# Kernel tuning notes

Measured on AMD Instinct MI355X. Metric: run time of the kernel, lower is better.

The kernel has to match this reference:

```python
import jax, jax.numpy as jnp
import numpy as np
import math

EPS = 1e-5
L2_EPS = 1e-12  # torch F.normalize default eps


def _bitlinear(x, W):
    """BitNet b1.58-style BitLinear: ternary weights (per-tensor mean-abs scale)
    and per-token int8 absmax activation quantization. No bias.
    x: [..., in], W: [out, in] -> [..., out]
    """
    w_scale = jnp.clip(jnp.mean(jnp.abs(W)), EPS, None)
    W_q = jnp.clip(jnp.round(W / w_scale), -1.0, 1.0) * w_scale
    x_scale = 127.0 / jnp.clip(jnp.max(jnp.abs(x), axis=-1, keepdims=True), EPS, None)
    x_q = jnp.clip(jnp.round(x * x_scale), -128.0, 127.0) / x_scale
    return jnp.einsum('bsi,oi->bso', x_q, W_q)


def setup_inputs() -> dict:
    key = jax.random.key(0)
    k1, k2, k3 = jax.random.split(key, 3)
    B, S, D_in, P, D_out = 4, 4096, 2048, 16, 2048
    x = jax.random.normal(k1, (B, S, D_in), dtype=jnp.float32)
    # xavier_normal_: std = sqrt(2 / (fan_in + fan_out))
    Wk = jax.random.normal(k2, (P, D_in), dtype=jnp.float32) * math.sqrt(2.0 / (D_in + P))
    Wv = jax.random.normal(k3, (D_out, P), dtype=jnp.float32) * math.sqrt(2.0 / (P + D_out))
    return {"x": x, "Wk": Wk, "Wv": Wv}


def reference(x, Wk, Wv):
    # key projection -> [B, S, P]
    attn = _bitlinear(x, Wk)
    # gelu (exact erf form, torch default) + L2-normalize * sqrt(P)
    attn = jax.nn.gelu(attn, approximate=False)
    norm = jnp.clip(jnp.linalg.norm(attn, axis=-1, keepdims=True), L2_EPS, None)
    attn = attn / norm * jnp.sqrt(jnp.float32(attn.shape[-1]))
    # value projection -> [B, S, D_out]
    return _bitlinear(attn, Wv)
```

## Files before the change

### kernel.cpp

```cpp
#include <hip/hip_runtime.h>

#define DIN   2048
#define DOUT  2048
#define NP    16
#define TPW   4
#define WPB   4

#define HDR_OFF   0
#define WK4_OFF   256
#define WV4_OFF   (WK4_OFF + 32768)

static __device__ __forceinline__ int dot4(unsigned a, unsigned b, int c) {
#if defined(__has_builtin) && __has_builtin(__builtin_amdgcn_sdot4)
  return __builtin_amdgcn_sdot4((int)a, (int)b, c, false);
#else
  c += (int)(signed char)(a & 0xffu)        * (int)(signed char)(b & 0xffu);
  c += (int)(signed char)((a >> 8) & 0xffu) * (int)(signed char)((b >> 8) & 0xffu);
  c += (int)(signed char)((a >> 16) & 0xffu)* (int)(signed char)((b >> 16) & 0xffu);
  c += (int)(signed char)(a >> 24)          * (int)(signed char)(b >> 24);
  return c;
#endif
}

static __device__ __forceinline__ unsigned qmagic(float f, float xs) {
  return __float_as_uint(fmaf(f, xs, 12582912.0f)) & 0xffu;
}

static __device__ __forceinline__ unsigned q8(float f, float xs) {
  float t = f * xs;
  float r = rintf(t);
  r = fmaxf(-128.0f, fminf(127.0f, r));
  return ((unsigned)(int)r) & 0xffu;
}

__global__ __launch_bounds__(256) void k_prep(
    const float* __restrict__ Wk, const float* __restrict__ Wv,
    float* __restrict__ hdr, unsigned* __restrict__ wk4, unsigned* __restrict__ wv4)
{
  __shared__ float red[8][256];
  const int tid = threadIdx.x, b = blockIdx.x;
  const int isV = (b >= 32);
  const float4* W = (const float4*)(isV ? Wv : Wk);

  float4 own = make_float4(0.f, 0.f, 0.f, 0.f);
#pragma unroll
  for (int lb = 0; lb < 8; ++lb) {
    float s = 0.f;
#pragma unroll
    for (int i = 0; i < 4; ++i) {
      float4 v = W[lb * 1024 + i * 256 + tid];
      if (!isV && (lb * 4 + i) == b) own = v;
      s += fabsf(v.x) + fabsf(v.y) + fabsf(v.z) + fabsf(v.w);
    }
    red[lb][tid] = s;
  }
  __syncthreads();
#pragma unroll 1
  for (int o = 128; o > 0; o >>= 1) {
    if (tid < o) {
#pragma unroll
      for (int lb = 0; lb < 8; ++lb) red[lb][tid] += red[lb][tid + o];
    }
    __syncthreads();
  }
  float sum = 0.f;
#pragma unroll
  for (int lb = 0; lb < 8; ++lb) sum += red[lb][0];
  const float sc = fmaxf(sum * (1.0f / 32768.0f), 1e-5f);
  if (tid == 0 && (b == 0 || b == 32)) hdr[isV] = sc;

  if (!isV) {
    const int c = b * 256 + tid;
    unsigned pk = 0; const float* wp = &own.x;
#pragma unroll
    for (int j = 0; j < 4; ++j) {
      float r = rintf(wp[j] / sc);
      r = fmaxf(-1.0f, fminf(1.0f, r));
      pk |= (((unsigned)(int)r) & 0xffu) << (8 * j);
    }
    wk4[c] = pk;
  } else {
    const int o = (b - 32) * 256 + tid;
    unsigned u[4];
#pragma unroll
    for (int cc = 0; cc < 4; ++cc) {
      float4 w = ((const float4*)Wv)[o * 4 + cc];
      const float* wp = &w.x;
      unsigned pk = 0;
#pragma unroll
      for (int r = 0; r < 4; ++r) {
        float q = rintf(wp[r] / sc);
        q = fmaxf(-1.0f, fminf(1.0f, q));
        pk |= (((unsigned)(int)q) & 0xffu) << (8 * r);
      }
      u[cc] = pk;
    }
    const int m = o >> 8, r = o & 255, lr = r >> 2, j = r & 3;
    ((uint4*)wv4)[(m * 4 + j) * 64 + lr] = make_uint4(u[0], u[1], u[2], u[3]);
  }
}

__global__ __launch_bounds__(256, 4) void k_main(
    const float* __restrict__ x, const float* __restrict__ hdr,
    const unsigned* __restrict__ wk4, const unsigned* __restrict__ wv4t,
    float* __restrict__ out)
{
  const int tid = threadIdx.x;
  const int l   = tid & 63;
  const int ws  = tid >> 6;
  const long t0 = ((long)blockIdx.x * WPB + ws) * TPW;

  __shared__ uint4 wkL[2048];
  __shared__ uint4 qls[WPB][TPW];
  __shared__ float sls[WPB][TPW];

  const float w1 = hdr[0], w2 = hdr[1];
  const float4* xf  = (const float4*)x;
  const uint4*  wvt = (const uint4*)wv4t;

#pragma unroll 1
  for (int r = 0; r < 8; ++r) {
    const int d = r * 256 + tid;
    const int p = d >> 7, half = (d >> 6) & 1, lg = d & 63;
    const int s = p * 512 + half * 256 + lg;
    wkL[d] = make_uint4(wk4[s], wk4[s + 64], wk4[s + 128], wk4[s + 192]);
  }
  __syncthreads();

#pragma unroll 1
  for (int t = 0; t < TPW; ++t) {
    const long tok = t0 + t;

    float4 a[8];
#pragma unroll
    for (int c = 0; c < 8; ++c) a[c] = xf[tok * 512 + c * 64 + l];

    float mx = 0.0f;
#pragma unroll
    for (int c = 0; c < 8; ++c) {
      mx = fmaxf(mx, fabsf(a[c].x)); mx = fmaxf(mx, fabsf(a[c].y));
      mx = fmaxf(mx, fabsf(a[c].z)); mx = fmaxf(mx, fabsf(a[c].w));
    }
#pragma unroll
    for (int d = 1; d < 64; d <<= 1) mx = fmaxf(mx, __shfl_xor(mx, d, 64));
    const float mcl = fmaxf(mx, 1e-5f);
    const float xs  = 127.0f / mcl;
    const float s1  = w1 / xs;

    unsigned qp[8];
#pragma unroll
    for (int c = 0; c < 8; ++c) {
      qp[c] = qmagic(a[c].x, xs) | (qmagic(a[c].y, xs) << 8)
            | (qmagic(a[c].z, xs) << 16) | (qmagic(a[c].w, xs) << 24);
    }

    int acc[16];
#pragma unroll
    for (int p = 0; p < 16; ++p) {
      const uint4 w0 = wkL[p * 128 + l];
      const uint4 w4 = wkL[p * 128 + 64 + l];
      int d = 0;
      d = dot4(qp[0], w0.x, d); d = dot4(qp[1], w0.y, d);
      d = dot4(qp[2], w0.z, d); d = dot4(qp[3], w0.w, d);
      d = dot4(qp[4], w4.x, d); d = dot4(qp[5], w4.y, d);
      d = dot4(qp[6], w4.z, d); d = dot4(qp[7], w4.w, d);
      acc[p] = d;
    }

#pragma unroll
    for (int b = 0; b < 4; ++b) {
      const int lb = (l >> b) & 1;
#pragma unroll
      for (int j = 0; j < 8; ++j) {
        if (j < (8 >> b)) {
          int keep = lb ? acc[2 * j + 1] : acc[2 * j];
          int send = lb ? acc[2 * j]     : acc[2 * j + 1];
          acc[j] = keep + __shfl_xor(send, 1 << b, 64);
        }
      }
    }
    int rr = acc[0];
    rr += __shfl_xor(rr, 16, 64);
    rr += __shfl_xor(rr, 32, 64);

    const float fa = (float)rr * s1;
    const float gv = 0.5f * fa * (1.0f + erff(fa * 0.70710678118654752f));
    float ss = gv * gv;
    ss += __shfl_xor(ss, 1, 64); ss += __shfl_xor(ss, 2, 64);
    ss += __shfl_xor(ss, 4, 64); ss += __shfl_xor(ss, 8, 64);
    const float rn = fmaxf(sqrtf(ss), 1e-12f);
    const float gn = gv * (4.0f / rn);
    float am = fabsf(gn);
    {
      float o;
      o = __shfl_xor(am, 1, 64); am = fmaxf(am, o);
      o = __shfl_xor(am, 2, 64); am = fmaxf(am, o);
      o = __shfl_xor(am, 4, 64); am = fmaxf(am, o);
      o = __shfl_xor(am, 8, 64); am = fmaxf(am, o);
    }
    const float mc2 = fmaxf(am, 1e-5f);
    const float xs2 = 127.0f / mc2;
    const float s2  = w2 / xs2;

    unsigned sh = q8(gn, xs2) << ((l & 3) * 8);
    sh |= (unsigned)__shfl_xor((int)sh, 1, 64);
    sh |= (unsigned)__shfl_xor((int)sh, 2, 64);
    const unsigned wa = (unsigned)__shfl_xor((int)sh, 4, 64);
    const unsigned wb = (unsigned)__shfl_xor((int)sh, 8, 64);
    const unsigned wc = (unsigned)__shfl_xor((int)sh, 12, 64);
    if (l == 0) {
      qls[ws][t] = make_uint4(sh, wa, wb, wc);
      sls[ws][t] = s2;
    }
  }

  uint4 q[TPW]; float s2v[TPW];
#pragma unroll
  for (int i = 0; i < TPW; ++i) { q[i] = qls[ws][i]; s2v[i] = sls[ws][i]; }

#pragma unroll 1
  for (int m = 0; m < 8; ++m) {
    const uint4 wv0 = wvt[(m * 4 + 0) * 64 + l];
    const uint4 wv1 = wvt[(m * 4 + 1) * 64 + l];
    const uint4 wv2 = wvt[(m * 4 + 2) * 64 + l];
    const uint4 wv3 = wvt[(m * 4 + 3) * 64 + l];
#pragma unroll
    for (int t = 0; t < TPW; ++t) {
      float h[4];
      {
        int d = dot4(q[t].x, wv0.x, 0);
        d = dot4(q[t].y, wv0.y, d); d = dot4(q[t].z, wv0.z, d);
        d = dot4(q[t].w, wv0.w, d); h[0] = (float)d * s2v[t];
      }
      {
        int d = dot4(q[t].x, wv1.x, 0);
        d = dot4(q[t].y, wv1.y, d); d = dot4(q[t].z, wv1.z, d);
        d = dot4(q[t].w, wv1.w, d); h[1] = (float)d * s2v[t];
      }
      {
        int d = dot4(q[t].x, wv2.x, 0);
        d = dot4(q[t].y, wv2.y, d); d = dot4(q[t].z, wv2.z, d);
        d = dot4(q[t].w, wv2.w, d); h[2] = (float)d * s2v[t];
      }
      {
        int d = dot4(q[t].x, wv3.x, 0);
        d = dot4(q[t].y, wv3.y, d); d = dot4(q[t].z, wv3.z, d);
        d = dot4(q[t].w, wv3.w, d); h[3] = (float)d * s2v[t];
      }
      *(float4*)(out + (size_t)(t0 + t) * 2048 + m * 256 + l * 4) =
          make_float4(h[0], h[1], h[2], h[3]);
    }
  }
}

extern "C" void kernel_launch(void* const* d_in, const int* in_sizes, int n_in,
                              void* d_out, int out_size, void* d_ws, size_t ws_size,
                              hipStream_t stream) {
  const float* x  = (const float*)d_in[0];
  const float* Wk = (const float*)d_in[1];
  const float* Wv = (const float*)d_in[2];

  const int tokens = in_sizes[0] / DIN;

  char* ws = (char*)d_ws;
  float*    hdr = (float*)(ws + HDR_OFF);
  unsigned* wk4 = (unsigned*)(ws + WK4_OFF);
  unsigned* wv4 = (unsigned*)(ws + WV4_OFF);

  k_prep<<<40, 256, 0, stream>>>(Wk, Wv, hdr, wk4, wv4);
  k_main<<<tokens / (TPW * WPB), 256, 0, stream>>>(x, hdr, wk4, wv4, (float*)d_out);
}
```

Measured before the change: 297.8 us.

## Split fused BitLinear kernel into quantize, key-projection and value-projection kernels

The single fused kernel is replaced by three kernels. The first quantizes x to int8 and writes the result plus per-token scales to workspace. The second computes the 16-wide key projection, GELU, normalization and requantization with a different thread mapping: per-thread partial dots are reduced through shared memory instead of many wave shuffles. The third computes the output projection with a separate grid over output column blocks. This adds a 32 MB int8 write and read-back of x plus two extra launches, in exchange for simpler, more parallel stages.

```diff
diff --git a/kernel.cpp b/kernel.cpp
--- a/kernel.cpp
+++ b/kernel.cpp
@@ -3,12 +3,14 @@
 #define DIN   2048
 #define DOUT  2048
 #define NP    16
-#define TPW   4
-#define WPB   4
 
 #define HDR_OFF   0
 #define WK4_OFF   256
 #define WV4_OFF   (WK4_OFF + 32768)
+#define XSW_OFF   (WV4_OFF + 32768)
+#define XQ_OFF    (XSW_OFF + 65536)
+#define Q2_OFF    (XQ_OFF + 33554432)
+#define S2_OFF    (Q2_OFF + 262144)
 
 static __device__ __forceinline__ int dot4(unsigned a, unsigned b, int c) {
 #if defined(__has_builtin) && __has_builtin(__builtin_amdgcn_sdot4)
@@ -100,37 +102,17 @@
   }
 }
 
-__global__ __launch_bounds__(256, 4) void k_main(
-    const float* __restrict__ x, const float* __restrict__ hdr,
-    const unsigned* __restrict__ wk4, const unsigned* __restrict__ wv4t,
-    float* __restrict__ out)
-{
-  const int tid = threadIdx.x;
-  const int l   = tid & 63;
-  const int ws  = tid >> 6;
-  const long t0 = ((long)blockIdx.x * WPB + ws) * TPW;
-
-  __shared__ uint4 wkL[2048];
-  __shared__ uint4 qls[WPB][TPW];
-  __shared__ float sls[WPB][TPW];
-
-  const float w1 = hdr[0], w2 = hdr[1];
-  const float4* xf  = (const float4*)x;
-  const uint4*  wvt = (const uint4*)wv4t;
-
-#pragma unroll 1
-  for (int r = 0; r < 8; ++r) {
-    const int d = r * 256 + tid;
-    const int p = d >> 7, half = (d >> 6) & 1, lg = d & 63;
-    const int s = p * 512 + half * 256 + lg;
-    wkL[d] = make_uint4(wk4[s], wk4[s + 64], wk4[s + 128], wk4[s + 192]);
-  }
-  __syncthreads();
-
-#pragma unroll 1
-  for (int t = 0; t < TPW; ++t) {
-    const long tok = t0 + t;
-
+__global__ __launch_bounds__(256) void k_quant(
+    const float* __restrict__ x, unsigned* __restrict__ xqw,
+    float* __restrict__ xsw)
+{
+  const int tid = threadIdx.x, l = tid & 63, wv = tid >> 6;
+  const long tb = (long)blockIdx.x * 16 + wv * 4;
+  const float4* xf = (const float4*)x;
+
+#pragma unroll 1
+  for (int i = 0; i < 4; ++i) {
+    const long tok = tb + i;
     float4 a[8];
 #pragma unroll
     for (int c = 0; c < 8; ++c) a[c] = xf[tok * 512 + c * 64 + l];
@@ -145,111 +127,133 @@
     for (int d = 1; d < 64; d <<= 1) mx = fmaxf(mx, __shfl_xor(mx, d, 64));
     const float mcl = fmaxf(mx, 1e-5f);
     const float xs  = 127.0f / mcl;
-    const float s1  = w1 / xs;
-
-    unsigned qp[8];
+
 #pragma unroll
     for (int c = 0; c < 8; ++c) {
-      qp[c] = qmagic(a[c].x, xs) | (qmagic(a[c].y, xs) << 8)
-            | (qmagic(a[c].z, xs) << 16) | (qmagic(a[c].w, xs) << 24);
-    }
-
-    int acc[16];
+      const unsigned q = qmagic(a[c].x, xs) | (qmagic(a[c].y, xs) << 8)
+                       | (qmagic(a[c].z, xs) << 16) | (qmagic(a[c].w, xs) << 24);
+      xqw[tok * 512 + c * 64 + l] = q;
+    }
+    if (l == 0) xsw[tok] = xs;
+  }
+}
+
+__global__ __launch_bounds__(256) void k_mid(
+    const unsigned* __restrict__ xq, const float* __restrict__ xsw,
+    const unsigned* __restrict__ wk4, const float* __restrict__ hdr,
+    uint4* __restrict__ q2w, float* __restrict__ s2w)
+{
+  __shared__ unsigned wkS[8192];
+  __shared__ int accS[4][32][17];
+
+  const int tid = threadIdx.x, l = tid & 63, wv = tid >> 6;
+  const long t0 = (long)blockIdx.x * 32;
+
+#pragma unroll 1
+  for (int i = 0; i < 32; ++i) wkS[i * 256 + tid] = wk4[i * 256 + tid];
+  __syncthreads();
+
+  const int t = l >> 1, h = l & 1;
+  const unsigned* xrow = xq + (t0 + t) * 512 + wv * 128 + h * 64;
+  const unsigned* wbase = wkS + wv * 128 + h * 64;
+
+  int acc[16];
+#pragma unroll
+  for (int p = 0; p < 16; ++p) acc[p] = 0;
+
+#pragma unroll 2
+  for (int c4 = 0; c4 < 16; ++c4) {
+    const uint4 xv = *(const uint4*)(xrow + c4 * 4);
 #pragma unroll
     for (int p = 0; p < 16; ++p) {
-      const uint4 w0 = wkL[p * 128 + l];
-      const uint4 w4 = wkL[p * 128 + 64 + l];
-      int d = 0;
-      d = dot4(qp[0], w0.x, d); d = dot4(qp[1], w0.y, d);
-      d = dot4(qp[2], w0.z, d); d = dot4(qp[3], w0.w, d);
-      d = dot4(qp[4], w4.x, d); d = dot4(qp[5], w4.y, d);
-      d = dot4(qp[6], w4.z, d); d = dot4(qp[7], w4.w, d);
+      const uint4 w = *(const uint4*)(wbase + p * 512 + c4 * 4);
+      int d = acc[p];
+      d = dot4(xv.x, w.x, d); d = dot4(xv.y, w.y, d);
+      d = dot4(xv.z, w.z, d); d = dot4(xv.w, w.w, d);
       acc[p] = d;
     }
-
-#pragma unroll
-    for (int b = 0; b < 4; ++b) {
-      const int lb = (l >> b) & 1;
-#pragma unroll
-      for (int j = 0; j < 8; ++j) {
-        if (j < (8 >> b)) {
-          int keep = lb ? acc[2 * j + 1] : acc[2 * j];
-          int send = lb ? acc[2 * j]     : acc[2 * j + 1];
-          acc[j] = keep + __shfl_xor(send, 1 << b, 64);
-        }
-      }
-    }
-    int rr = acc[0];
-    rr += __shfl_xor(rr, 16, 64);
-    rr += __shfl_xor(rr, 32, 64);
-
-    const float fa = (float)rr * s1;
-    const float gv = 0.5f * fa * (1.0f + erff(fa * 0.70710678118654752f));
-    float ss = gv * gv;
-    ss += __shfl_xor(ss, 1, 64); ss += __shfl_xor(ss, 2, 64);
-    ss += __shfl_xor(ss, 4, 64); ss += __shfl_xor(ss, 8, 64);
-    const float rn = fmaxf(sqrtf(ss), 1e-12f);
-    const float gn = gv * (4.0f / rn);
-    float am = fabsf(gn);
-    {
-      float o;
-      o = __shfl_xor(am, 1, 64); am = fmaxf(am, o);
-      o = __shfl_xor(am, 2, 64); am = fmaxf(am, o);
-      o = __shfl_xor(am, 4, 64); am = fmaxf(am, o);
-      o = __shfl_xor(am, 8, 64); am = fmaxf(am, o);
-    }
+  }
+
+#pragma unroll
+  for (int p = 0; p < 16; ++p) acc[p] += __shfl_xor(acc[p], 1, 64);
+  if (h == 0) {
+#pragma unroll
+    for (int p = 0; p < 16; ++p) accS[wv][t][p] = acc[p];
+  }
+  __syncthreads();
+
+  if (tid < 32) {
+    const long tok = t0 + tid;
+    int r[16];
+#pragma unroll
+    for (int p = 0; p < 16; ++p)
+      r[p] = ((accS[0][tid][p] + accS[1][tid][p]) + accS[2][tid][p]) + accS[3][tid][p];
+
+    const float xs = xsw[tok];
+    const float s1 = hdr[0] / xs;
+
+    float g[16];
+#pragma unroll
+    for (int p = 0; p < 16; ++p) {
+      const float fa = (float)r[p] * s1;
+      g[p] = 0.5f * fa * (1.0f + erff(fa * 0.70710678118654752f));
+    }
+    float t1[8], t2[4], t3[2];
+#pragma unroll
+    for (int j = 0; j < 8; ++j) t1[j] = g[2 * j] * g[2 * j] + g[2 * j + 1] * g[2 * j + 1];
+#pragma unroll
+    for (int j = 0; j < 4; ++j) t2[j] = t1[2 * j] + t1[2 * j + 1];
+    t3[0] = t2[0] + t2[1]; t3[1] = t2[2] + t2[3];
+    const float ssum = t3[0] + t3[1];
+
+    const float rn  = fmaxf(sqrtf(ssum), 1e-12f);
+    const float inv = 4.0f / rn;
+    float gn[16]; float am = 0.0f;
+#pragma unroll
+    for (int p = 0; p < 16; ++p) { gn[p] = g[p] * inv; am = fmaxf(am, fabsf(gn[p])); }
     const float mc2 = fmaxf(am, 1e-5f);
     const float xs2 = 127.0f / mc2;
-    const float s2  = w2 / xs2;
-
-    unsigned sh = q8(gn, xs2) << ((l & 3) * 8);
-    sh |= (unsigned)__shfl_xor((int)sh, 1, 64);
-    sh |= (unsigned)__shfl_xor((int)sh, 2, 64);
-    const unsigned wa = (unsigned)__shfl_xor((int)sh, 4, 64);
-    const unsigned wb = (unsigned)__shfl_xor((int)sh, 8, 64);
-    const unsigned wc = (unsigned)__shfl_xor((int)sh, 12, 64);
-    if (l == 0) {
-      qls[ws][t] = make_uint4(sh, wa, wb, wc);
-      sls[ws][t] = s2;
-    }
-  }
-
-  uint4 q[TPW]; float s2v[TPW];
-#pragma unroll
-  for (int i = 0; i < TPW; ++i) { q[i] = qls[ws][i]; s2v[i] = sls[ws][i]; }
-
-#pragma unroll 1
-  for (int m = 0; m < 8; ++m) {
-    const uint4 wv0 = wvt[(m * 4 + 0) * 64 + l];
-    const uint4 wv1 = wvt[(m * 4 + 1) * 64 + l];
-    const uint4 wv2 = wvt[(m * 4 + 2) * 64 + l];
-    const uint4 wv3 = wvt[(m * 4 + 3) * 64 + l];
-#pragma unroll
-    for (int t = 0; t < TPW; ++t) {
-      float h[4];
-      {
-        int d = dot4(q[t].x, wv0.x, 0);
-        d = dot4(q[t].y, wv0.y, d); d = dot4(q[t].z, wv0.z, d);
-        d = dot4(q[t].w, wv0.w, d); h[0] = (float)d * s2v[t];
-      }
-      {
-        int d = dot4(q[t].x, wv1.x, 0);
-        d = dot4(q[t].y, wv1.y, d); d = dot4(q[t].z, wv1.z, d);
-        d = dot4(q[t].w, wv1.w, d); h[1] = (float)d * s2v[t];
-      }
-      {
-        int d = dot4(q[t].x, wv2.x, 0);
-        d = dot4(q[t].y, wv2.y, d); d = dot4(q[t].z, wv2.z, d);
-        d = dot4(q[t].w, wv2.w, d); h[2] = (float)d * s2v[t];
-      }
-      {
-        int d = dot4(q[t].x, wv3.x, 0);
-        d = dot4(q[t].y, wv3.y, d); d = dot4(q[t].z, wv3.z, d);
-        d = dot4(q[t].w, wv3.w, d); h[3] = (float)d * s2v[t];
-      }
-      *(float4*)(out + (size_t)(t0 + t) * 2048 + m * 256 + l * 4) =
-          make_float4(h[0], h[1], h[2], h[3]);
-    }
+    const float s2  = hdr[1] / xs2;
+
+    unsigned w[4];
+#pragma unroll
+    for (int j = 0; j < 4; ++j)
+      w[j] = q8(gn[4 * j], xs2)            | (q8(gn[4 * j + 1], xs2) << 8)
+           | (q8(gn[4 * j + 2], xs2) << 16) | (q8(gn[4 * j + 3], xs2) << 24);
+    q2w[tok] = make_uint4(w[0], w[1], w[2], w[3]);
+    s2w[tok] = s2;
+  }
+}
+
+__global__ __launch_bounds__(256) void k_out(
+    const uint4* __restrict__ wv4t, const uint4* __restrict__ q2w,
+    const float* __restrict__ s2w, float* __restrict__ out)
+{
+  const int tid = threadIdx.x, l = tid & 63, wv = tid >> 6;
+  const int m = blockIdx.x & 7;
+  const long tb = (long)(blockIdx.x >> 3) * 64 + wv * 16;
+
+  const uint4 w0 = wv4t[(m * 4 + 0) * 64 + l];
+  const uint4 w1 = wv4t[(m * 4 + 1) * 64 + l];
+  const uint4 w2 = wv4t[(m * 4 + 2) * 64 + l];
+  const uint4 w3 = wv4t[(m * 4 + 3) * 64 + l];
+
+#pragma unroll 1
+  for (int i = 0; i < 16; ++i) {
+    const long tok = tb + i;
+    const uint4 q  = q2w[tok];
+    const float s2 = s2w[tok];
+    int d; float h0, h1, h2, h3;
+    d = dot4(q.x, w0.x, 0); d = dot4(q.y, w0.y, d);
+    d = dot4(q.z, w0.z, d); d = dot4(q.w, w0.w, d); h0 = (float)d * s2;
+    d = dot4(q.x, w1.x, 0); d = dot4(q.y, w1.y, d);
+    d = dot4(q.z, w1.z, d); d = dot4(q.w, w1.w, d); h1 = (float)d * s2;
+    d = dot4(q.x, w2.x, 0); d = dot4(q.y, w2.y, d);
+    d = dot4(q.z, w2.z, d); d = dot4(q.w, w2.w, d); h2 = (float)d * s2;
+    d = dot4(q.x, w3.x, 0); d = dot4(q.y, w3.y, d);
+    d = dot4(q.z, w3.z, d); d = dot4(q.w, w3.w, d); h3 = (float)d * s2;
+    *(float4*)(out + (size_t)tok * 2048 + m * 256 + l * 4) =
+        make_float4(h0, h1, h2, h3);
   }
 }
 
@@ -266,7 +270,14 @@
   float*    hdr = (float*)(ws + HDR_OFF);
   unsigned* wk4 = (unsigned*)(ws + WK4_OFF);
   unsigned* wv4 = (unsigned*)(ws + WV4_OFF);
-
-  k_prep<<<40, 256, 0, stream>>>(Wk, Wv, hdr, wk4, wv4);
-  k_main<<<tokens / (TPW * WPB), 256, 0, stream>>>(x, hdr, wk4, wv4, (float*)d_out);
-}
+  float*    xsw = (float*)(ws + XSW_OFF);
+  unsigned* xqw = (unsigned*)(ws + XQ_OFF);
+  uint4*    q2w = (uint4*)(ws + Q2_OFF);
+  float*    s2w = (float*)(ws + S2_OFF);
+
+  k_prep <<<40, 256, 0, stream>>>(Wk, Wv, hdr, wk4, wv4);
+  k_quant<<<tokens / 16, 256, 0, stream>>>(x, xqw, xsw);
+  k_mid  <<<tokens / 32, 256, 0, stream>>>(xqw, xsw, wk4, hdr, q2w, s2w);
+  k_out  <<<(tokens / 64) * 8, 256, 0, stream>>>((const uint4*)wv4, q2w, s2w,
+                                                 (float*)d_out);
+}
```

New measurement: 274.1 us. 1.09x faster.
